# Kernel optimization log

Hardware: AMD Instinct MI355X
Metric: run time of the kernel (lower is better)

Reference implementation:

```python
import jax, jax.numpy as jnp
import numpy as np

# ---- module hyperparameters (init_kwargs) ----
QMIN, QMAX, QBINS = -8.0, 8.0, 128
PMIN, PMAX, PBINS = -10.0, 10.0, 128
GAMMA_F = 1.0
N_TRAJ = 16384


def _grid():
    # x = arange(qmin - 4/gamma_f, qmax + 4/gamma_f + 0.1/maxp, 0.1/maxp)
    maxp = max(abs(PMIN), abs(PMAX))
    step = 0.1 / maxp
    x = np.arange(QMIN - 4.0 / GAMMA_F, QMAX + 4.0 / GAMMA_F + step, step)
    return x.astype(np.float32)


def setup_inputs() -> dict:
    key = jax.random.key(0)
    ks = jax.random.split(key, 6)
    shape = (1, N_TRAJ)
    x = jnp.asarray(_grid())
    # psi buffer: stand-in for np.interp(x, spl.x, spl.psis[-1][1]) -- a
    # localized oscillatory wavefunction sampled on the grid.
    psi = (jnp.exp(-0.5 * (x - 1.0) ** 2) * jnp.cos(2.0 * x)).astype(jnp.float32)
    return {
        "factors_re": jax.random.normal(ks[0], shape, jnp.float32),
        "factors_im": jax.random.normal(ks[1], shape, jnp.float32),
        "q_re": jax.random.normal(ks[2], shape, jnp.float32),
        "q_im": 0.5 * jax.random.normal(ks[3], shape, jnp.float32),
        "p_re": jax.random.normal(ks[4], shape, jnp.float32),
        "p_im": 0.5 * jax.random.normal(ks[5], shape, jnp.float32),
        "x": x,
        "psi": psi,
    }


def _trapz0(y, x):
    # trapezoid rule along axis 0; y: [M, N] (complex), x: [M]
    dx = jnp.diff(x)
    return jnp.sum(0.5 * (y[1:] + y[:-1]) * dx[:, None], axis=0)


def _forward(factors_re, factors_im, q_re, q_im, p_re, p_im, x, psi):
    g = GAMMA_F
    factors = factors_re + 1j * factors_im  # [1, N] complex
    # _calc_proj: xi = 2*g*q + 1j*p ; qf = Re(xi)/(2g), pf = Im(xi)
    qf = q_re - p_im / (2.0 * g)
    pf = 2.0 * g * q_im + p_re
    dq = (QMAX - QMIN) / QBINS
    dp = (PMAX - PMIN) / PBINS
    qb = jnp.floor((qf - QMIN) / dq)
    pb = jnp.floor((pf - PMIN) / dp)
    bins = (qb * PBINS + pb).astype(jnp.int32).reshape(-1)  # [N]
    n = bins.shape[0]
    # torch: enumerate(torch.unique(bins)) -> rank among sorted unique values.
    # jnp.unique inverse (size=n, large fill pads at the end) gives the same map.
    _, inv = jnp.unique(bins, return_inverse=True, size=n, fill_value=jnp.int32(2**30))
    inds = inv.reshape(qf.shape)  # [1, N] compact bin ids
    qc = (qb + 0.5) * dq + QMIN  # bin centers [1, N]
    pc = (pb + 0.5) * dp + PMIN
    # _gf: coherent-state Gaussians on grid x -> [M, N]
    norm = (2.0 * g / jnp.pi) ** 0.25
    dxq = x[:, None] - qc.reshape(-1)[None, :]  # [M, N]
    gfs = norm * jnp.exp(-g * dxq * dxq + 1j * pc.reshape(-1)[None, :] * dxq)
    gt = _trapz0(jnp.conj(gfs) * psi[:, None], x)  # [N] complex
    # _calc_pref (reconstruction): exponential prefactor that can blow up,
    # hence the nan_to_num + clamp in the original.
    pref = norm * jnp.exp(g * q_im * q_im + 1j * (p_re * q_im))  # [1, N]
    pref = (jnp.clip(jnp.nan_to_num(pref.real), -100.0, 100.0)
            + 1j * jnp.clip(jnp.nan_to_num(pref.imag), -100.0, 100.0))
    vals = pref * factors  # [1, N]
    b = vals.shape[0]
    binned = jnp.zeros_like(vals).at[jnp.arange(b)[:, None], inds].add(vals)
    loss = jnp.sum(jnp.abs(binned - gt[None, :]) ** 2)
    return jnp.sqrt(loss)


def reference(factors_re, factors_im, q_re, q_im, p_re, p_im, x, psi):
    return _forward(factors_re, factors_im, q_re, q_im, p_re, p_im, x, psi)
```

## Files before the change

### kernel.cpp

```cpp
#include <hip/hip_runtime.h>
#include <math.h>


#define PRES_WORDS 1024
#define PRES_BITS  65536
#define PRES_OFF   32768
#define CHUNKS     8
#define MCAP       2432
#define WINR       3.5f
#define NORM       0.8932438417380023f

__global__ void __launch_bounds__(256) gt_kernel(
    const float* __restrict__ q_re, const float* __restrict__ q_im,
    const float* __restrict__ p_re, const float* __restrict__ p_im,
    const float* __restrict__ x, const float* __restrict__ psi,
    unsigned long long* __restrict__ pres,
    float* __restrict__ bre, float* __restrict__ bim,
    float* __restrict__ gpre, float* __restrict__ gpim, int n, int M)
{
    __shared__ float swpsi[MCAP];
    int tid = threadIdx.x;
    float x0 = x[0];
    float h  = x[1] - x0;
    for (int m = tid; m < M; m += 256) {
        float w = (m == 0 || m == M - 1) ? 0.5f * h : h;
        swpsi[m] = w * psi[m] * NORM;
    }
    __syncthreads();
    int t = blockIdx.x * 256 + tid;
    if (t >= n) return;
    float qi = q_im[t], pr = p_re[t];
    float qf = q_re[t] - 0.5f * p_im[t];
    float pf = 2.0f * qi + pr;
    float qb = floorf((qf + 8.0f) / 0.125f);
    float pb = floorf((pf + 10.0f) / 0.15625f);
    float qcn = (qb + 0.5f) * 0.125f - 8.0f;
    float pcn = (pb + 0.5f) * 0.15625f - 10.0f;
    if (blockIdx.y == 0) {
        int b = (int)(qb * 128.0f + pb);
        int pidx = min(max(b + PRES_OFF, 0), PRES_BITS - 1);
        atomicOr(&pres[pidx >> 6], 1ull << (pidx & 63));
        bre[t] = 0.0f; bim[t] = 0.0f;
    }
    float inv_h = 1.0f / h;
    int mlo = max(0, (int)((qcn - WINR - x0) * inv_h) - 1);
    int mhi = min(M, (int)((qcn + WINR - x0) * inv_h) + 2);
    int len = mhi - mlo; if (len < 0) len = 0;
    int c = blockIdx.y;
    int ms = mlo + (len * c) / CHUNKS;
    int me = mlo + (len * (c + 1)) / CHUNKS;
    float dx0 = fmaf((float)ms, h, x0 - qcn);
    float e   = __expf(-dx0 * dx0);
    float u   = __expf(-h * (dx0 + dx0 + h));
    float d   = __expf(-2.0f * h * h);
    float sn, cs, sd, cd;
    __sincosf(pcn * dx0, &sn, &cs);
    __sincosf(pcn * h, &sd, &cd);
    float sre = 0.0f, sim = 0.0f;
    for (int m = ms; m < me; m++) {
        float w = swpsi[m];
        float tv = e * w;
        sre = fmaf(tv, cs, sre);
        sim = fmaf(-tv, sn, sim);
        e *= u; u *= d;
        float cn = fmaf(cs, cd, -sn * sd);
        sn = fmaf(sn, cd, cs * sd);
        cs = cn;
    }
    gpre[c * n + t] = sre;
    gpim[c * n + t] = sim;
}

__global__ void __launch_bounds__(256) scatter_loss_kernel(
    const float* __restrict__ f_re, const float* __restrict__ f_im,
    const float* __restrict__ q_re, const float* __restrict__ q_im,
    const float* __restrict__ p_re, const float* __restrict__ p_im,
    const unsigned long long* __restrict__ pres,
    float* __restrict__ bre, float* __restrict__ bim,
    const float* __restrict__ gpre, const float* __restrict__ gpim,
    int* __restrict__ k3done, float* __restrict__ loss, int* __restrict__ fin,
    float* __restrict__ out, int n)
{
    __shared__ int lbase[PRES_WORDS];
    int tid = threadIdx.x;
    if (tid < 64) {
        int cum[16];
        int tot = 0;
        for (int k = 0; k < 16; k++) { cum[k] = tot; tot += __popcll(pres[tid * 16 + k]); }
        int run = tot;
        for (int off = 1; off < 64; off <<= 1) {
            int up = __shfl_up(run, off);
            if (tid >= off) run += up;
        }
        int excl = run - tot;
        for (int k = 0; k < 16; k++) lbase[tid * 16 + k] = excl + cum[k];
    }
    __syncthreads();
    int t = blockIdx.x * 256 + tid;
    float sre = 0.0f, sim = 0.0f;
    for (int c = 0; c < CHUNKS; c++) {
        sre += gpre[c * n + t];
        sim += gpim[c * n + t];
    }
    float qi = q_im[t], pr = p_re[t];
    float qf = q_re[t] - 0.5f * p_im[t];
    float pf = 2.0f * qi + pr;
    float qb = floorf((qf + 8.0f) / 0.125f);
    float pb = floorf((pf + 10.0f) / 0.15625f);
    int b = (int)(qb * 128.0f + pb);
    int pidx = min(max(b + PRES_OFF, 0), PRES_BITS - 1);
    int w = pidx >> 6, bit = pidx & 63;
    unsigned long long below = pres[w] & ((bit == 0) ? 0ull : (~0ull >> (64 - bit)));
    int cid = lbase[w] + __popcll(below);
    float ea = NORM * expf(qi * qi);
    float s, c2;
    __sincosf(pr * qi, &s, &c2);
    float prr = fminf(fmaxf(ea * c2, -100.0f), 100.0f);
    float pri = fminf(fmaxf(ea * s, -100.0f), 100.0f);
    float fr = f_re[t], fi = f_im[t];
    atomicAdd(&bre[cid], prr * fr - pri * fi);
    atomicAdd(&bim[cid], prr * fi + pri * fr);
    __threadfence();
    __syncthreads();
    if (tid == 0) {
        __hip_atomic_fetch_add(k3done, 1, __ATOMIC_ACQ_REL, __HIP_MEMORY_SCOPE_AGENT);
        while (__hip_atomic_load(k3done, __ATOMIC_ACQUIRE, __HIP_MEMORY_SCOPE_AGENT)
               < (int)gridDim.x)
            __builtin_amdgcn_s_sleep(4);
    }
    __syncthreads();
    float brt  = __hip_atomic_load(&bre[t], __ATOMIC_RELAXED, __HIP_MEMORY_SCOPE_AGENT);
    float bit2 = __hip_atomic_load(&bim[t], __ATOMIC_RELAXED, __HIP_MEMORY_SCOPE_AGENT);
    float dre = brt - sre;
    float dim = bit2 - sim;
    float v = dre * dre + dim * dim;
#pragma unroll
    for (int off = 32; off > 0; off >>= 1) v += __shfl_down(v, off);
    __shared__ float l[4];
    int wv = tid >> 6, ln = tid & 63;
    if (ln == 0) l[wv] = v;
    __syncthreads();
    if (tid == 0) {
        __hip_atomic_fetch_add(loss, l[0] + l[1] + l[2] + l[3],
                               __ATOMIC_ACQ_REL, __HIP_MEMORY_SCOPE_AGENT);
        int old = __hip_atomic_fetch_add(fin, 1, __ATOMIC_ACQ_REL,
                                         __HIP_MEMORY_SCOPE_AGENT);
        if (old == (int)gridDim.x - 1) {
            out[0] = sqrtf(__hip_atomic_load(loss, __ATOMIC_ACQUIRE,
                                             __HIP_MEMORY_SCOPE_AGENT));
        }
    }
}

extern "C" void kernel_launch(void* const* d_in, const int* in_sizes, int n_in,
                              void* d_out, int out_size, void* d_ws, size_t ws_size,
                              hipStream_t stream)
{
    const float* f_re = (const float*)d_in[0];
    const float* f_im = (const float*)d_in[1];
    const float* q_re = (const float*)d_in[2];
    const float* q_im = (const float*)d_in[3];
    const float* p_re = (const float*)d_in[4];
    const float* p_im = (const float*)d_in[5];
    const float* x    = (const float*)d_in[6];
    const float* psi  = (const float*)d_in[7];
    int n = in_sizes[0];
    int M = in_sizes[6];

    float* gpre = (float*)d_ws;
    float* gpim = gpre + (size_t)CHUNKS * n;
    float* bre  = gpim + (size_t)CHUNKS * n;
    float* bim  = bre + n;
    unsigned long long* pres = (unsigned long long*)(bim + n);
    float* loss    = (float*)(pres + PRES_WORDS);
    int*   k3done  = (int*)(loss + 1);
    int*   fin     = k3done + 1;

    hipMemsetAsync(pres, 0, PRES_WORDS * sizeof(unsigned long long) + 12, stream);

    int nb = (n + 255) / 256;
    gt_kernel<<<dim3(nb, CHUNKS), 256, 0, stream>>>(q_re, q_im, p_re, p_im, x, psi,
                                                    pres, bre, bim, gpre, gpim, n, M);
    scatter_loss_kernel<<<nb, 256, 0, stream>>>(f_re, f_im, q_re, q_im, p_re, p_im,
                                                pres, bre, bim, gpre, gpim,
                                                k3done, loss, fin, (float*)d_out, n);
}
```

Measured before the change: 106.9 us.

## Fold Gaussian and phase into one complex recurrence, vectorize psi loads, double chunks

The trapezoid inner loop now carries a single complex phasor z = e·exp(-i·p·dx) multiplied by a complex step W that decays by d each iteration, replacing the separate real-exponential and rotation updates. The window is aligned to multiples of four so psi weights are read from shared memory as float4, with the table zero-padded up to MCAP. The chunk count along the grid rises from 8 to 16 to expose more parallelism per trajectory. In exchange the window widens slightly, and the scatter kernel must re-add twice as many partial sums from global memory.

```diff
diff --git a/kernel.cpp b/kernel.cpp
--- a/kernel.cpp
+++ b/kernel.cpp
@@ -5,7 +5,7 @@
 #define PRES_WORDS 1024
 #define PRES_BITS  65536
 #define PRES_OFF   32768
-#define CHUNKS     8
+#define CHUNKS     16
 #define MCAP       2432
 #define WINR       3.5f
 #define NORM       0.8932438417380023f
@@ -18,13 +18,17 @@
     float* __restrict__ bre, float* __restrict__ bim,
     float* __restrict__ gpre, float* __restrict__ gpim, int n, int M)
 {
-    __shared__ float swpsi[MCAP];
+    __shared__ __align__(16) float swpsi[MCAP];
     int tid = threadIdx.x;
     float x0 = x[0];
     float h  = x[1] - x0;
-    for (int m = tid; m < M; m += 256) {
-        float w = (m == 0 || m == M - 1) ? 0.5f * h : h;
-        swpsi[m] = w * psi[m] * NORM;
+    for (int m = tid; m < MCAP; m += 256) {
+        float v = 0.0f;
+        if (m < M) {
+            float w = (m == 0 || m == M - 1) ? 0.5f * h : h;
+            v = w * psi[m] * NORM;
+        }
+        swpsi[m] = v;
     }
     __syncthreads();
     int t = blockIdx.x * 256 + tid;
@@ -43,12 +47,13 @@
         bre[t] = 0.0f; bim[t] = 0.0f;
     }
     float inv_h = 1.0f / h;
-    int mlo = max(0, (int)((qcn - WINR - x0) * inv_h) - 1);
+    int mlo = max(0, (int)((qcn - WINR - x0) * inv_h) - 1) & ~3;
     int mhi = min(M, (int)((qcn + WINR - x0) * inv_h) + 2);
-    int len = mhi - mlo; if (len < 0) len = 0;
+    mhi = (mhi + 3) & ~3;
+    int G = (mhi - mlo) >> 2; if (G < 0) G = 0;
     int c = blockIdx.y;
-    int ms = mlo + (len * c) / CHUNKS;
-    int me = mlo + (len * (c + 1)) / CHUNKS;
+    int ms = mlo + (((G * c) >> 4) << 2);
+    int me = mlo + (((G * (c + 1)) >> 4) << 2);
     float dx0 = fmaf((float)ms, h, x0 - qcn);
     float e   = __expf(-dx0 * dx0);
     float u   = __expf(-h * (dx0 + dx0 + h));
@@ -56,17 +61,21 @@
     float sn, cs, sd, cd;
     __sincosf(pcn * dx0, &sn, &cs);
     __sincosf(pcn * h, &sd, &cd);
+    float zre = e * cs,  zim = -e * sn;
+    float Wre = u * cd,  Wim = -u * sd;
     float sre = 0.0f, sim = 0.0f;
-    for (int m = ms; m < me; m++) {
-        float w = swpsi[m];
-        float tv = e * w;
-        sre = fmaf(tv, cs, sre);
-        sim = fmaf(-tv, sn, sim);
-        e *= u; u *= d;
-        float cn = fmaf(cs, cd, -sn * sd);
-        sn = fmaf(sn, cd, cs * sd);
-        cs = cn;
+#define STEP(WV) {                                   \
+        sre = fmaf((WV), zre, sre);                  \
+        sim = fmaf((WV), zim, sim);                  \
+        float zt = fmaf(zre, Wre, -(zim * Wim));     \
+        zim = fmaf(zre, Wim, zim * Wre);             \
+        zre = zt;                                    \
+        Wre *= d; Wim *= d; }
+    for (int m = ms; m < me; m += 4) {
+        float4 wv = *(const float4*)(swpsi + m);
+        STEP(wv.x) STEP(wv.y) STEP(wv.z) STEP(wv.w)
     }
+#undef STEP
     gpre[c * n + t] = sre;
     gpim[c * n + t] = sim;
 }
```

Measured after the change: 110.5 us. +3.4%, slower.
